# Performance work log

Hardware: AMD Instinct MI355X
Metric: run time of the kernel (lower is better)

The kernel has to match this reference:

```python
import jax, jax.numpy as jnp
import numpy as np

B, V, H, W = 1, 88, 128, 256
P = 2                  # patch size
D = 128                # hidden_dim = embed_dim // latent_ratio = 1536 // 12
NG = 12                # n_group (== latent_ratio)
NH = 2                 # heads per attention = num_heads // latent_ratio = 24 // 12
E = NG * D             # embed_dim = 1536
HD = D // NH
SCALE = HD ** -0.5

# Static ragged group index sets derived from the variable names (sizes 7,7,7,7,7,9,9,9,9,9,17,6).
# Pressure-level vars are ordered z,q,t,u,v per level; levels [50..400]=7 levels, [50..600]=9 levels.
_off = {'z': 0, 'q': 1, 't': 2, 'u': 3, 'v': 4}
GROUPS = []
for name in ['u1', 'v1', 't1', 'q1', 'z1', 'u2', 'v2', 't2', 'q2', 'z2', 'surf', 'const']:
    if name[-1] in '12':
        nl = 7 if name[-1] == '1' else 9
        GROUPS.append(np.array([5 * li + _off[name[0]] for li in range(nl)]))
    elif name == 'surf':
        GROUPS.append(np.arange(65, 82))   # 17 surface vars
    else:
        GROUPS.append(np.arange(82, 88))   # 6 constant vars


def setup_inputs() -> dict:
    key = jax.random.key(0)
    ks = jax.random.split(key, 16)
    return {
        "x": jax.random.normal(ks[0], (B, V, H, W), jnp.float32),
        # per-variable conv patch-embed weights, flattened to (V, P*P, D)
        "conv_w": jax.random.normal(ks[1], (V, P * P, D), jnp.float32) * 0.05,
        "conv_b": jax.random.normal(ks[2], (V, D), jnp.float32) * 0.02,
        "channel_embed": jax.random.normal(ks[3], (1, V, D), jnp.float32) * 0.02,
        "channel_query": jax.random.uniform(ks[4], (1, NG, D), jnp.float32) * 0.2,
        # 12 distinct MultiheadAttention modules: packed in_proj (3D, D) + out_proj
        "grp_in_w": jax.random.normal(ks[5], (NG, 3 * D, D), jnp.float32) * 0.05,
        "grp_in_b": jax.random.normal(ks[6], (NG, 3 * D), jnp.float32) * 0.02,
        "grp_out_w": jax.random.normal(ks[7], (NG, D, D), jnp.float32) * 0.05,
        "grp_out_b": jax.random.normal(ks[8], (NG, D), jnp.float32) * 0.02,
        "ens_query": jax.random.uniform(ks[9], (1, NG, D), jnp.float32) * 0.2,
        "ens_in_w": jax.random.normal(ks[10], (3 * D, D), jnp.float32) * 0.05,
        "ens_in_b": jax.random.normal(ks[11], (3 * D,), jnp.float32) * 0.02,
        "ens_out_w": jax.random.normal(ks[12], (D, D), jnp.float32) * 0.05,
        "ens_out_b": jax.random.normal(ks[13], (D,), jnp.float32) * 0.02,
        "ln_gamma": jnp.ones((E,), jnp.float32),
        "ln_beta": jnp.zeros((E,), jnp.float32),
    }


def reference(x, conv_w, conv_b, channel_embed, channel_query,
              grp_in_w, grp_in_b, grp_out_w, grp_out_b,
              ens_query, ens_in_w, ens_in_b, ens_out_w, ens_out_b,
              ln_gamma, ln_beta):
    b, v, h, w = x.shape
    hp, wp = h // P, w // P
    L = hp * wp
    # non-overlapping stride-P conv with 1 input channel == patchify + per-variable matmul
    patches = x.reshape(b, v, hp, P, wp, P).transpose(0, 1, 2, 4, 3, 5).reshape(b, v, L, P * P)
    xe = jnp.einsum('bvlp,vpd->bvld', patches, conv_w) + conv_b[None, :, None, :]
    xe = xe + channel_embed[:, :, None, :]                 # (B, V, L, D)
    xn = xe.transpose(0, 2, 1, 3).reshape(b * L, v, D)     # (N, V, D), N = B*L

    outs = []
    for i, ids in enumerate(GROUPS):                       # 12 fixed, structurally distinct groups
        kv = xn[:, ids, :]                                 # (N, g, D), ragged g
        Wq, Wk, Wv = grp_in_w[i, :D], grp_in_w[i, D:2 * D], grp_in_w[i, 2 * D:]
        bq, bk, bv = grp_in_b[i, :D], grp_in_b[i, D:2 * D], grp_in_b[i, 2 * D:]
        q = (channel_query[0, i] @ Wq.T + bq).reshape(NH, HD)
        k = (kv @ Wk.T + bk).reshape(-1, len(ids), NH, HD)
        vv = (kv @ Wv.T + bv).reshape(-1, len(ids), NH, HD)
        a = jax.nn.softmax(jnp.einsum('hd,nghd->nhg', q, k) * SCALE, axis=-1)
        o = jnp.einsum('nhg,nghd->nhd', a, vv).reshape(-1, D)
        outs.append(o @ grp_out_w[i].T + grp_out_b[i])
    out = jnp.stack(outs, axis=1)                          # (N, 12, D)

    Wq, Wk, Wv = ens_in_w[:D], ens_in_w[D:2 * D], ens_in_w[2 * D:]
    bq, bk, bv = ens_in_b[:D], ens_in_b[D:2 * D], ens_in_b[2 * D:]
    q = (ens_query[0] @ Wq.T + bq).reshape(NG, NH, HD)     # 12 ensemble query tokens
    k = (out @ Wk.T + bk).reshape(-1, NG, NH, HD)
    vv = (out @ Wv.T + bv).reshape(-1, NG, NH, HD)
    a = jax.nn.softmax(jnp.einsum('thd,nshd->nhts', q, k) * SCALE, axis=-1)
    r = jnp.einsum('nhts,nshd->nthd', a, vv).reshape(-1, NG, D)
    r = (r @ ens_out_w.T + ens_out_b).reshape(b, L, E)     # (B, L, embed_dim)

    mu = r.mean(axis=-1, keepdims=True)
    var = r.var(axis=-1, keepdims=True)
    return (r - mu) * jax.lax.rsqrt(var + 1e-5) * ln_gamma + ln_beta
```

## Files before the change

### kernel.cpp

```cpp
#include <hip/hip_runtime.h>


typedef __attribute__((ext_vector_type(8))) short short8;
typedef __attribute__((ext_vector_type(4))) float f32x4;

__constant__ int GOFF[13] = {0,7,14,21,28,35,44,53,62,71,80,97,103};
__constant__ int K5A[12]  = {35,35,35,35,35,45,45,45,45,45,85,30};
__constant__ int SLOTS3[12] = {3,3,3,3,3,3,3,3,3,3,6,2};
__constant__ int FOFFA[12] = {0,3,6,9,12,15,18,21,24,27,30,36};
__constant__ int GSLOT[103] = {
  3,8,13,18,23,28,33,
  4,9,14,19,24,29,34,
  2,7,12,17,22,27,32,
  1,6,11,16,21,26,31,
  0,5,10,15,20,25,30,
  3,8,13,18,23,28,33,38,43,
  4,9,14,19,24,29,34,39,44,
  2,7,12,17,22,27,32,37,42,
  1,6,11,16,21,26,31,36,41,
  0,5,10,15,20,25,30,35,40,
  45,46,47,48,49,50,51,52,53,54,55,56,57,58,59,60,61,
  62,63,64,65,66,67};
__constant__ int GIDX[103] = {
  0,0,0,0,0,0,0, 1,1,1,1,1,1,1, 2,2,2,2,2,2,2, 3,3,3,3,3,3,3, 4,4,4,4,4,4,4,
  5,5,5,5,5,5,5,5,5, 6,6,6,6,6,6,6,6,6, 7,7,7,7,7,7,7,7,7, 8,8,8,8,8,8,8,8,8,
  9,9,9,9,9,9,9,9,9,
  10,10,10,10,10,10,10,10,10,10,10,10,10,10,10,10,10,
  11,11,11,11,11,11};

constexpr int cSLOTS[12] = {3,3,3,3,3,3,3,3,3,3,6,2};
constexpr int cFOFFA[12] = {0,3,6,9,12,15,18,21,24,27,30,36};

#define QK_GRP 0
#define QK_ENS 3072
#define QB_GRP 6144
#define QB_ENS 6176
#define CGRP   6208
#define CENS   7744
#define CWQ_BYTE   43776
#define MPL_BYTE   50432
#define MEB_BYTE   1623296
#define QKEB_BYTE  1688832
#define FWS_BYTE   1697024

__device__ __forceinline__ float bf2f(unsigned short s) {
  return __uint_as_float(((unsigned)s) << 16);
}
__device__ __forceinline__ unsigned short f2bf(float f) {
  unsigned u = __float_as_uint(f);
  u += 0x7fffu + ((u >> 16) & 1u);
  return (unsigned short)(u >> 16);
}

__global__ void hwe_p1(const float* __restrict__ giw, const float* __restrict__ gib,
                       const float* __restrict__ gow, const float* __restrict__ gob,
                       const float* __restrict__ cq,  const float* __restrict__ eq,
                       const float* __restrict__ eiw, const float* __restrict__ eib,
                       const float* __restrict__ eow, const float* __restrict__ eob,
                       float* __restrict__ wsf, float* __restrict__ Mplain,
                       unsigned short* __restrict__ MeB, unsigned short* __restrict__ Fws) {
  int blk = blockIdx.x, tid = threadIdx.x;
  int wave = tid >> 6, lane = tid & 63;
  if (blk < 48) {
    __shared__ float qf[64];
    bool ens = blk >= 24;
    int bi = ens ? blk - 24 : blk;
    int i = bi >> 1, h = bi & 1;
    const float* W  = ens ? eiw : giw + i*49152;
    const float* bv = ens ? eib : gib + i*384;
    const float* qv = ens ? eq + i*128 : cq + i*128;
    for (int it = 0; it < 16; ++it) {
      int dp = it*4 + wave;
      const float* wrow = W + (h*64 + dp)*128;
      float acc = wrow[lane]*qv[lane] + wrow[lane+64]*qv[lane+64];
#pragma unroll
      for (int off = 32; off > 0; off >>= 1) acc += __shfl_down(acc, off);
      if (lane == 0) qf[dp] = acc + bv[h*64 + dp];
    }
    __syncthreads();
    if (tid < 128) {
      int e = tid;
      const float* Wk = W + (128 + h*64)*128 + e;
      float a0=0.f,a1=0.f,a2=0.f,a3=0.f;
      for (int dp = 0; dp < 64; dp += 4) {
        a0 += qf[dp+0] * Wk[(dp+0)*128];
        a1 += qf[dp+1] * Wk[(dp+1)*128];
        a2 += qf[dp+2] * Wk[(dp+2)*128];
        a3 += qf[dp+3] * Wk[(dp+3)*128];
      }
      wsf[(ens ? QK_ENS : QK_GRP) + bi*128 + e] = (a0+a1)+(a2+a3);
    }
    if (wave == 3) {
      float acc = qf[lane] * bv[128 + h*64 + lane];
#pragma unroll
      for (int off = 32; off > 0; off >>= 1) acc += __shfl_down(acc, off);
      if (lane == 0) wsf[(ens ? QB_ENS : QB_GRP) + bi] = acc;
    }
  } else if (blk < 1584) {
    int b2 = blk - 48;
    int gi = b2 >> 7, r = b2 & 127;
    int ep = tid, h = ep >> 7, e = ep & 127;
    const float* wo = gow + gi*16384 + r*128 + h*64;
    const float* wv = giw + gi*49152 + (256 + h*64)*128 + e;
    float a0=0.f,a1=0.f,a2=0.f,a3=0.f;
    for (int hd = 0; hd < 64; hd += 4) {
      a0 += wo[hd+0] * wv[(hd+0)*128];
      a1 += wo[hd+1] * wv[(hd+1)*128];
      a2 += wo[hd+2] * wv[(hd+2)*128];
      a3 += wo[hd+3] * wv[(hd+3)*128];
    }
    Mplain[(gi*128 + r)*256 + ep] = (a0+a1)+(a2+a3);
  } else if (blk < 1712) {
    int f2 = (blk - 1584)*256 + tid;
    int r = f2 >> 8, ep = f2 & 255;
    int h = ep >> 7, e = ep & 127;
    const float* wo = eow + r*128 + h*64;
    const float* wv = eiw + (256 + h*64)*128 + e;
    float a0=0.f,a1=0.f,a2=0.f,a3=0.f;
    for (int hd = 0; hd < 64; hd += 4) {
      a0 += wo[hd+0] * wv[(hd+0)*128];
      a1 += wo[hd+1] * wv[(hd+1)*128];
      a2 += wo[hd+2] * wv[(hd+2)*128];
      a3 += wo[hd+3] * wv[(hd+3)*128];
    }
    float acc = (a0+a1)+(a2+a3);
    int mt = r >> 4, lr = r & 15, kt = ep >> 5, q = (ep >> 3) & 3, j = ep & 7;
    MeB[((mt*8 + kt)*64 + (q*16 + lr))*8 + j] = f2bf(acc);
  } else if (blk < 2096) {
    int id = (blk - 1712)*4 + wave;
    int i = id >> 7, d = id & 127;
    const float* wrow = gow + i*16384 + d*128;
    const float* bvv = gib + i*384 + 256;
    float acc = wrow[lane]*bvv[lane] + wrow[lane+64]*bvv[lane+64];
#pragma unroll
    for (int off = 32; off > 0; off >>= 1) acc += __shfl_down(acc, off);
    if (lane == 0) wsf[CGRP + id] = acc + gob[i*128 + d];
  } else if (blk < 2128) {
    int d = (blk - 2096)*4 + wave;
    const float* wrow = eow + d*128;
    const float* bvv = eib + 256;
    float acc = wrow[lane]*bvv[lane] + wrow[lane+64]*bvv[lane+64];
#pragma unroll
    for (int off = 32; off > 0; off >>= 1) acc += __shfl_down(acc, off);
    if (lane == 0) wsf[CENS + d] = acc + eob[d];
  } else {
    int idx = (blk - 2128)*256 + tid;
    if (idx < 19456) ((uint4*)Fws)[idx] = (uint4){0,0,0,0};
  }
}

__global__ void hwe_p2(const float* __restrict__ cw, const float* __restrict__ cb,
                       const float* __restrict__ ce, const float* __restrict__ Mplain,
                       const float* __restrict__ wsf,
                       unsigned short* __restrict__ Fws,
                       unsigned short* __restrict__ qkeB, float* __restrict__ cwq) {
  int blk = blockIdx.x, tid = threadIdx.x;
  if (blk < 192) {
    __shared__ __align__(16) unsigned short M16[16*130];
    __shared__ __align__(16) unsigned short cwl[85*130];
    int gi = blk >> 4, h = (blk >> 3) & 1, mt = blk & 7;
    int go = GOFF[gi], K5 = K5A[gi], S = SLOTS3[gi];
    int r0 = mt*16;
    for (int idx = tid; idx < 2048; idx += 256) {
      int rr = idx >> 7, e = idx & 127;
      M16[rr*130 + e] = f2bf(Mplain[(gi*128 + r0 + rr)*256 + h*128 + e]);
    }
    for (int idx = tid; idx < K5*128; idx += 256) {
      int k = idx >> 7, e = idx & 127;
      int q = (k*205) >> 10;
      int pp = k - q*5;
      int s = GSLOT[go + q];
      int v = (s < 45) ? s : s + 20;
      float val = (pp < 4) ? cw[(v*4 + pp)*128 + e] : (cb[v*128 + e] + ce[v*128 + e]);
      cwl[k*130 + e] = f2bf(val);
    }
    __syncthreads();
    const unsigned* M32 = (const unsigned*)M16;
    const unsigned* C32 = (const unsigned*)cwl;
    for (int o = tid; o < 16*K5; o += 256) {
      int k = o >> 4, rr = o & 15;
      float acc = 0.f;
#pragma unroll 8
      for (int e2 = 0; e2 < 64; ++e2) {
        unsigned m = M32[rr*65 + e2];
        unsigned c = C32[k*65 + e2];
        acc += __uint_as_float(m << 16) * __uint_as_float(c << 16);
        acc += __uint_as_float(m & 0xffff0000u) * __uint_as_float(c & 0xffff0000u);
      }
      int kpp = h*K5 + k;
      int ktl = kpp >> 5;
      int addr = (FOFFA[gi]*8 + mt*S + ktl)*512 + ((kpp >> 3) & 3)*128 + rr*8 + (kpp & 7);
      Fws[addr] = f2bf(acc);
    }
  } else if (blk < 208) {
    int f4 = (blk - 192)*256 + tid;
    int lane = (f4 >> 3) & 63, j = f4 & 7;
    int th = ((f4 >> 11) & 1)*16 + (lane & 15);
    int kt = (f4 >> 9) & 3;
    float val = (th < 24) ? wsf[QK_ENS + th*128 + kt*32 + (lane >> 4)*8 + j] : 0.f;
    qkeB[f4] = f2bf(val);
  } else {
    int wid = (blk - 208)*4 + (tid >> 6);
    int lane = tid & 63;
    if (wid < 206) {
      int gg = wid >> 1, h = wid & 1;
      int gi = GIDX[gg];
      int s = GSLOT[gg];
      int v = (s < 45) ? s : s + 20;
      const float* qk = wsf + QK_GRP + (gi*2 + h)*128;
      float q0 = qk[lane], q1 = qk[lane + 64];
      float a[5];
#pragma unroll
      for (int pp = 0; pp < 4; ++pp)
        a[pp] = cw[(v*4 + pp)*128 + lane]*q0 + cw[(v*4 + pp)*128 + lane + 64]*q1;
      a[4] = (cb[v*128 + lane] + ce[v*128 + lane])*q0 +
             (cb[v*128 + lane + 64] + ce[v*128 + lane + 64])*q1;
#pragma unroll
      for (int off = 32; off > 0; off >>= 1)
#pragma unroll
        for (int kk = 0; kk < 5; ++kk) a[kk] += __shfl_down(a[kk], off);
      if (lane == 0) {
        float* o = cwq + (gg*2 + h)*8;
        o[0] = a[0]*0.125f; o[1] = a[1]*0.125f; o[2] = a[2]*0.125f; o[3] = a[3]*0.125f;
        o[4] = (a[4] + wsf[QB_GRP + gi*2 + h]) * 0.125f;
      }
    }
  }
}

__global__ __launch_bounds__(256, 3) void hwe_main(
    const float* __restrict__ x,
    const float* __restrict__ lgam, const float* __restrict__ lbet,
    const float* __restrict__ wsf,  const float* __restrict__ cwq,
    const unsigned short* __restrict__ Fws, const unsigned short* __restrict__ MeB,
    const unsigned short* __restrict__ qkeB,
    float* __restrict__ out) {
  __shared__ __align__(16) unsigned char smem[53632];
  unsigned short* xpB   = (unsigned short*)(smem);
  unsigned short* scb   = (unsigned short*)(smem + 4352);
  unsigned short* wpAll = (unsigned short*)(smem + 7680);
  unsigned short* Gl    = (unsigned short*)(smem);
  unsigned short* apB   = (unsigned short*)(smem + 20480);
  unsigned short* sce2  = (unsigned short*)(smem);
  unsigned short* outg2 = (unsigned short*)(smem + 28672);
  float*          stats = (float*)(smem + 53504);

  const int tid  = threadIdx.x;
  const int wave = tid >> 6;
  const int lane = tid & 63;
  const int quad = lane >> 4;
  const int l15  = lane & 15;

  const int hi   = blockIdx.x >> 4;
  const int wib  = (blockIdx.x & 15) << 3;
  const int nbase = hi*128 + wib;

  for (int idx = tid; idx < 1088; idx += 256) {
    int c2 = idx & 7, r = (idx >> 3) & 1, s = idx >> 4;
    int v = (s < 45) ? s : s + 20;
    const float2 xv = *(const float2*)(x + (v*128 + 2*hi + r)*256 + 2*wib + c2*2);
    unsigned pk = (unsigned)f2bf(xv.x) | ((unsigned)f2bf(xv.y) << 16);
    *(unsigned*)(xpB + (c2*68 + s)*4 + r*2) = pk;
  }
  if (tid < 64) ((unsigned*)outg2)[96*64 + tid] = 0u;
  __syncthreads();

  for (int idx = tid; idx < 1648; idx += 256) {
    int h = idx & 1, p = (idx >> 1) & 7, gg = idx >> 4;
    int s = GSLOT[gg];
    const float* c = cwq + (gg*2 + h)*8;
    const unsigned short* xr = xpB + (p*68 + s)*4;
    float acc = c[4] + bf2f(xr[0])*c[0] + bf2f(xr[1])*c[1]
                     + bf2f(xr[2])*c[2] + bf2f(xr[3])*c[3];
    scb[(p*2 + h)*104 + gg] = f2bf(acc);
  }
  __syncthreads();

  if (tid < 192) {
    int gi = tid % 12, h = (tid / 12) & 1, p = tid / 24;
    int go = GOFF[gi], G = GOFF[gi+1] - go;
    unsigned short* row = scb + (p*2 + h)*104 + go;
    float ev[17];
    float m = -1e30f;
#pragma unroll
    for (int g = 0; g < 17; ++g) {
      ev[g] = (g < G) ? bf2f(row[g]) : -1e30f;
      m = fmaxf(m, ev[g]);
    }
    float ssum = 0.f;
#pragma unroll
    for (int g = 0; g < 17; ++g) {
      float e = __expf(ev[g] - m);
      ev[g] = e;
      if (g < G) ssum += e;
    }
    float inv = 1.f / ssum;
#pragma unroll
    for (int g = 0; g < 17; ++g)
      if (g < G) row[g] = f2bf(ev[g] * inv);
  }
  __syncthreads();

#pragma unroll
  for (int hb = 0; hb < 2; ++hb) {
    const int nsl = hb ? 20 : 18;
    const int sbase = hb ? 18 : 0;

    short8 fA[6], fB[6];
    float4 cgA, cgB;
    auto fws_issue = [&](int I, short8 (&buf)[6], float4& cg) {
      int gi = hb*6 + (I >> 1);
      int S  = cSLOTS[gi];
      int mt = (I & 1)*4 + wave;
      const unsigned short* fp = Fws + (cFOFFA[gi]*8 + mt*S)*512 + lane*8;
#pragma unroll
      for (int kt = 0; kt < 6; ++kt)
        if (kt < S) buf[kt] = *(const short8*)(fp + kt*512);
      cg = *(const float4*)(wsf + CGRP + gi*128 + mt*16 + quad*4);
    };
    auto fws_compute = [&](int I, short8 (&buf)[6], const float4& cg) {
      int gi = hb*6 + (I >> 1);
      int S  = cSLOTS[gi];
      int mt = (I & 1)*4 + wave;
      int lbase = cFOFFA[gi] - sbase;
      f32x4 acc = {0.f,0.f,0.f,0.f};
#pragma unroll
      for (int kt = 0; kt < 6; ++kt)
        if (kt < S) {
          short8 b = *(const short8*)(wpAll + (lbase + kt)*512 + lane*8);
          acc = __builtin_amdgcn_mfma_f32_16x16x32_bf16(buf[kt], b, acc, 0, 0, 0);
        }
      if (l15 < 8) {
        int p = l15;
        int rb = mt*16 + quad*4;
        unsigned short t0 = f2bf(acc[0] + cg.x);
        unsigned short t1 = f2bf(acc[1] + cg.y);
        unsigned short t2 = f2bf(acc[2] + cg.z);
        unsigned short t3 = f2bf(acc[3] + cg.w);
        uint2 w;
        w.x = (unsigned)t0 | ((unsigned)t1 << 16);
        w.y = (unsigned)t2 | ((unsigned)t3 << 16);
        int row = gi*8 + p;
        int ch = (rb >> 3) ^ ((gi ^ p) & 7);
        *(uint2*)(outg2 + row*128 + ch*8 + (rb & 7)) = w;
      }
    };

    fws_issue(0, fA, cgA);

    {
      const int nposs = nsl * 512;
      for (int pos = tid*4; pos < nposs; pos += 1024) {
        int pf = (pos >> 3) & 15;
        uint2 w2 = {0u, 0u};
        if (pf < 8) {
          int ls = pos >> 9;
          int qd = (pos >> 7) & 3;
          int j0 = pos & 7;
          int p  = pf;
          int gil, K5, fo, goffB, c0, stp;
          if (hb == 0) {
            gil = (ls>=3)+(ls>=6)+(ls>=9)+(ls>=12)+(ls>=15);
            K5 = (gil < 5) ? 35 : 45;
            fo = gil*3;
            goffB = gil*7;
            c0 = (gil==0)?3:(gil==1)?4:(gil==2)?2:(gil==3)?1:(gil==4)?0:3;
            stp = 5;
          } else {
            gil = (ls>=3)+(ls>=6)+(ls>=9)+(ls>=12)+(ls>=18);
            K5 = (gil < 4) ? 45 : (gil == 4) ? 85 : 30;
            fo = (gil < 5) ? gil*3 : 18;
            goffB = (gil < 5) ? (44 + gil*9) : 97;
            c0 = (gil==0)?4:(gil==1)?2:(gil==2)?1:(gil==3)?0:(gil==4)?45:62;
            stp = (gil < 4) ? 5 : 1;
          }
          int kbase = (ls - fo)*32 + qd*8 + j0;
          unsigned short vv[4];
#pragma unroll
          for (int jj = 0; jj < 4; ++jj) {
            int kpp = kbase + jj;
            int h = (kpp >= K5) ? 1 : 0;
            int k = kpp - (h ? K5 : 0);
            int q = (k*205) >> 10;
            int pp = k - q*5;
            int gg = goffB + q;
            int s = c0 + q*stp;
            float a  = bf2f(scb[(p*2 + h)*104 + gg]);
            float xv = bf2f(xpB[(p*68 + s)*4 + pp]);
            float val = (pp < 4) ? a * xv : a;
            if (kpp >= 2*K5) val = 0.f;
            vv[jj] = f2bf(val);
          }
          w2.x = (unsigned)vv[0] | ((unsigned)vv[1] << 16);
          w2.y = (unsigned)vv[2] | ((unsigned)vv[3] << 16);
        }
        *(uint2*)(wpAll + pos) = w2;
      }
    }
    __syncthreads();

#pragma unroll
    for (int ii = 0; ii < 6; ++ii) {
      fws_issue(ii*2 + 1, fB, cgB);
      fws_compute(ii*2, fA, cgA);
      if (ii < 5) fws_issue(ii*2 + 2, fA, cgA);
      fws_compute(ii*2 + 1, fB, cgB);
    }
    __syncthreads();
  }

#pragma unroll
  for (int ti = 0; ti < 3; ++ti) {
    int T = wave*3 + ti;
    int mtp = T >> 1, ntp = T & 1;
    int rowA = mtp*16 + l15;
    int sx = ((rowA >> 3) ^ rowA) & 7;
    f32x4 acc = {0.f,0.f,0.f,0.f};
#pragma unroll
    for (int kt = 0; kt < 4; ++kt) {
      short8 a = *(const short8*)(outg2 + rowA*128 + (((kt*4 + quad) ^ sx) << 3));
      short8 b = *(const short8*)(qkeB + ((ntp*4 + kt)*64 + lane)*8);
      acc = __builtin_amdgcn_mfma_f32_16x16x32_bf16(a, b, acc, 0, 0, 0);
    }
    int th = ntp*16 + l15;
    if (th < 24) {
      float qb = wsf[QB_ENS + th];
#pragma unroll
      for (int reg = 0; reg < 4; ++reg) {
        int rowE = mtp*16 + quad*4 + reg;
        sce2[((rowE & 7)*24 + th)*16 + (rowE >> 3)] = f2bf((acc[reg] + qb) * 0.125f);
      }
    }
  }
  __syncthreads();

  if (tid < 192) {
    unsigned short* row = sce2 + tid*16;
    float ev[12];
    float m = -1e30f;
#pragma unroll
    for (int s = 0; s < 12; ++s) { ev[s] = bf2f(row[s]); m = fmaxf(m, ev[s]); }
    float ssum = 0.f;
#pragma unroll
    for (int s = 0; s < 12; ++s) { float e = __expf(ev[s] - m); ev[s] = e; ssum += e; }
    float inv = 1.f / ssum;
#pragma unroll
    for (int s = 0; s < 12; ++s) row[s] = f2bf(ev[s] * inv);
  }
  __syncthreads();

  for (int idx = tid; idx < 4096; idx += 256) {
    int p = idx >> 9, r9 = idx & 511;
    int ln = r9 >> 3, j = r9 & 7;
    int t = ln & 15, qd = ln >> 4;
    int kpp = qd*8 + j;
    int h = kpp >> 4, s = kpp & 15;
    unsigned short v = 0;
    if (s < 12 && t < 12) v = sce2[(p*24 + t*2 + h)*16 + s];
    apB[p*512 + ln*8 + j] = v;
  }
  float cens0[4], cens1[4];
  {
    float4 c0 = *(const float4*)(wsf + CENS + (wave*2 + 0)*16 + quad*4);
    float4 c1 = *(const float4*)(wsf + CENS + (wave*2 + 1)*16 + quad*4);
    cens0[0]=c0.x; cens0[1]=c0.y; cens0[2]=c0.z; cens0[3]=c0.w;
    cens1[0]=c1.x; cens1[1]=c1.y; cens1[2]=c1.z; cens1[3]=c1.w;
  }
  short8 meAr[16];
#pragma unroll
  for (int mi = 0; mi < 2; ++mi)
#pragma unroll
    for (int h = 0; h < 2; ++h)
#pragma unroll
      for (int kt = 0; kt < 4; ++kt)
        meAr[(mi*2 + h)*4 + kt] =
          *(const short8*)(MeB + (((wave*2 + mi)*8 + h*4 + kt)*64 + lane)*8);
  __syncthreads();

  for (int pp2 = 0; pp2 < 4; ++pp2) {
    f32x4 g[2][2][2];
#pragma unroll
    for (int lp = 0; lp < 2; ++lp)
#pragma unroll
      for (int mi = 0; mi < 2; ++mi)
#pragma unroll
        for (int h = 0; h < 2; ++h) g[lp][mi][h] = (f32x4){0.f,0.f,0.f,0.f};
#pragma unroll
    for (int lp = 0; lp < 2; ++lp) {
      int p = pp2*2 + lp;
      int brow = (l15 < 12) ? (l15*8 + p) : 96;
      int sx = ((brow >> 3) ^ brow) & 7;
#pragma unroll
      for (int h = 0; h < 2; ++h) {
#pragma unroll
        for (int kt = 0; kt < 4; ++kt) {
          short8 b = *(const short8*)(outg2 + brow*128 + (((kt*4 + quad) ^ sx) << 3));
          g[lp][0][h] = __builtin_amdgcn_mfma_f32_16x16x32_bf16(
              meAr[(0*2 + h)*4 + kt], b, g[lp][0][h], 0, 0, 0);
          g[lp][1][h] = __builtin_amdgcn_mfma_f32_16x16x32_bf16(
              meAr[(1*2 + h)*4 + kt], b, g[lp][1][h], 0, 0, 0);
        }
      }
    }
#pragma unroll
    for (int lp = 0; lp < 2; ++lp)
#pragma unroll
      for (int mi = 0; mi < 2; ++mi)
#pragma unroll
        for (int h = 0; h < 2; ++h)
#pragma unroll
          for (int reg = 0; reg < 4; ++reg) {
            int r = (wave*2 + mi)*16 + quad*4 + reg;
            Gl[lp*5120 + r*40 + h*16 + l15] = f2bf(g[lp][mi][h][reg]);
          }

    f32x4 rr[2][2];
    float s1[2] = {0.f, 0.f}, s2[2] = {0.f, 0.f};
#pragma unroll
    for (int lp = 0; lp < 2; ++lp) {
      int p = pp2*2 + lp;
      short8 bfrag = *(const short8*)(apB + p*512 + lane*8);
#pragma unroll
      for (int mi = 0; mi < 2; ++mi) {
        int mt2 = wave*2 + mi;
        short8 afrag = *(const short8*)(Gl + lp*5120 + (mt2*16 + l15)*40 + quad*8);
        f32x4 acc = {0.f,0.f,0.f,0.f};
        acc = __builtin_amdgcn_mfma_f32_16x16x32_bf16(afrag, bfrag, acc, 0, 0, 0);
#pragma unroll
        for (int reg = 0; reg < 4; ++reg)
          acc[reg] += (mi ? cens1[reg] : cens0[reg]);
        rr[lp][mi] = acc;
        if (l15 < 12) {
#pragma unroll
          for (int reg = 0; reg < 4; ++reg) {
            float v = acc[reg];
            s1[lp] += v; s2[lp] += v*v;
          }
        }
      }
    }
#pragma unroll
    for (int off = 32; off > 0; off >>= 1) {
#pragma unroll
      for (int lp = 0; lp < 2; ++lp) {
        s1[lp] += __shfl_xor(s1[lp], off);
        s2[lp] += __shfl_xor(s2[lp], off);
      }
    }
    int sb = (pp2 & 1) << 4;
    if (lane == 0) {
#pragma unroll
      for (int lp = 0; lp < 2; ++lp) {
        stats[sb + lp*4 + wave] = s1[lp];
        stats[sb + 8 + lp*4 + wave] = s2[lp];
      }
    }
    __syncthreads();
#pragma unroll
    for (int lp = 0; lp < 2; ++lp) {
      float t1 = stats[sb+lp*4+0] + stats[sb+lp*4+1] + stats[sb+lp*4+2] + stats[sb+lp*4+3];
      float t2 = stats[sb+8+lp*4+0] + stats[sb+8+lp*4+1] + stats[sb+8+lp*4+2] + stats[sb+8+lp*4+3];
      float mean = t1 * (1.f/1536.f);
      float var  = t2 * (1.f/1536.f) - mean*mean;
      float rstd = rsqrtf(var + 1e-5f);
      if (l15 < 12) {
        long nrow = (long)(nbase + pp2*2 + lp) * 1536;
#pragma unroll
        for (int mi = 0; mi < 2; ++mi) {
          int rb = (wave*2 + mi)*16 + quad*4;
          int j = l15*128 + rb;
          float4 gm = *(const float4*)(lgam + j);
          float4 bt = *(const float4*)(lbet + j);
          float4 o;
          o.x = (rr[lp][mi][0] - mean)*rstd*gm.x + bt.x;
          o.y = (rr[lp][mi][1] - mean)*rstd*gm.y + bt.y;
          o.z = (rr[lp][mi][2] - mean)*rstd*gm.z + bt.z;
          o.w = (rr[lp][mi][3] - mean)*rstd*gm.w + bt.w;
          *(float4*)(out + nrow + j) = o;
        }
      }
    }
  }
}

extern "C" void kernel_launch(void* const* d_in, const int* in_sizes, int n_in,
                              void* d_out, int out_size, void* d_ws, size_t ws_size,
                              hipStream_t stream) {
  const float* x   = (const float*)d_in[0];
  const float* cw  = (const float*)d_in[1];
  const float* cb  = (const float*)d_in[2];
  const float* ce  = (const float*)d_in[3];
  const float* cq  = (const float*)d_in[4];
  const float* giw = (const float*)d_in[5];
  const float* gib = (const float*)d_in[6];
  const float* gow = (const float*)d_in[7];
  const float* gob = (const float*)d_in[8];
  const float* eq  = (const float*)d_in[9];
  const float* eiw = (const float*)d_in[10];
  const float* eib = (const float*)d_in[11];
  const float* eow = (const float*)d_in[12];
  const float* eob = (const float*)d_in[13];
  const float* lg  = (const float*)d_in[14];
  const float* lb  = (const float*)d_in[15];

  float* wsf = (float*)d_ws;
  float* cwq = (float*)((char*)d_ws + CWQ_BYTE);
  float* Mplain = (float*)((char*)d_ws + MPL_BYTE);
  unsigned short* MeB  = (unsigned short*)((char*)d_ws + MEB_BYTE);
  unsigned short* qkeB = (unsigned short*)((char*)d_ws + QKEB_BYTE);
  unsigned short* Fws  = (unsigned short*)((char*)d_ws + FWS_BYTE);

  hwe_p1<<<2204, 256, 0, stream>>>(giw, gib, gow, gob, cq, eq, eiw, eib, eow, eob,
                                   wsf, Mplain, MeB, Fws);
  hwe_p2<<<260, 256, 0, stream>>>(cw, cb, ce, Mplain, wsf, Fws, qkeB, cwq);
  hwe_main<<<1024, 256, 0, stream>>>(x, lg, lb, wsf, cwq, Fws, MeB, qkeB,
                                     (float*)d_out);
}
```

Baseline: 205.1 us.

## Compute fused weight product in p2 with bf16 MFMA using pre-swizzled operands

The first kernel now writes the Wo·Wv product directly as bf16 in an MFMA-fragment layout and packs the gathered conv weights and biases into bf16 B-tiles. The second kernel then replaces its LDS staging and scalar bf16 dot-product loop with 16x16x32 bf16 MFMA instructions reading those tiles straight from global memory. This removes shared-memory staging, the barrier and scalar FMA work in the weight-folding stage, in exchange for 38 extra blocks in the first kernel. The main kernel, which likely dominates total time, is unchanged.

```diff
diff --git a/kernel.cpp b/kernel.cpp
--- a/kernel.cpp
+++ b/kernel.cpp
@@ -27,6 +27,10 @@
   9,9,9,9,9,9,9,9,9,
   10,10,10,10,10,10,10,10,10,10,10,10,10,10,10,10,10,
   11,11,11,11,11,11};
+__constant__ int TGI[38] = {0,0,0,1,1,1,2,2,2,3,3,3,4,4,4,5,5,5,6,6,6,7,7,7,
+                            8,8,8,9,9,9,10,10,10,10,10,10,11,11};
+__constant__ int TNT[38] = {0,1,2,0,1,2,0,1,2,0,1,2,0,1,2,0,1,2,0,1,2,0,1,2,
+                            0,1,2,0,1,2,0,1,2,3,4,5,0,1};
 
 constexpr int cSLOTS[12] = {3,3,3,3,3,3,3,3,3,3,6,2};
 constexpr int cFOFFA[12] = {0,3,6,9,12,15,18,21,24,27,30,36};
@@ -39,6 +43,7 @@
 #define CENS   7744
 #define CWQ_BYTE   43776
 #define MPL_BYTE   50432
+#define CW2_BYTE   836864
 #define MEB_BYTE   1623296
 #define QKEB_BYTE  1688832
 #define FWS_BYTE   1697024
@@ -57,7 +62,10 @@
                        const float* __restrict__ cq,  const float* __restrict__ eq,
                        const float* __restrict__ eiw, const float* __restrict__ eib,
                        const float* __restrict__ eow, const float* __restrict__ eob,
-                       float* __restrict__ wsf, float* __restrict__ Mplain,
+                       const float* __restrict__ cw,  const float* __restrict__ cb,
+                       const float* __restrict__ ce,
+                       float* __restrict__ wsf, unsigned short* __restrict__ MA,
+                       unsigned short* __restrict__ CW2,
                        unsigned short* __restrict__ MeB, unsigned short* __restrict__ Fws) {
   int blk = blockIdx.x, tid = threadIdx.x;
   int wave = tid >> 6, lane = tid & 63;
@@ -109,7 +117,9 @@
       a2 += wo[hd+2] * wv[(hd+2)*128];
       a3 += wo[hd+3] * wv[(hd+3)*128];
     }
-    Mplain[(gi*128 + r)*256 + ep] = (a0+a1)+(a2+a3);
+    float acc = (a0+a1)+(a2+a3);
+    int mt = r >> 4, lr = r & 15, kt = e >> 5, q = (e >> 3) & 3, j = e & 7;
+    MA[(((gi*2 + h)*8 + mt)*4 + kt)*512 + (q*16 + lr)*8 + j] = f2bf(acc);
   } else if (blk < 1712) {
     int f2 = (blk - 1584)*256 + tid;
     int r = f2 >> 8, ep = f2 & 255;
@@ -143,65 +153,89 @@
 #pragma unroll
     for (int off = 32; off > 0; off >>= 1) acc += __shfl_down(acc, off);
     if (lane == 0) wsf[CENS + d] = acc + eob[d];
+  } else if (blk < 2166) {
+    int tile = blk - 2128;
+    int gi = TGI[tile], nt = TNT[tile];
+    int kt = tid >> 6;
+    int l15b = tid & 15, quadb = (tid >> 4) & 3;
+    int k = nt*16 + l15b;
+    int e = kt*32 + quadb*8;
+    unsigned short vv[8];
+    if (k < K5A[gi]) {
+      int q = (k*205) >> 10;
+      int pp = k - q*5;
+      int s = GSLOT[GOFF[gi] + q];
+      int v = (s < 45) ? s : s + 20;
+      if (pp < 4) {
+        const float* src = cw + (v*4 + pp)*128 + e;
+#pragma unroll
+        for (int j = 0; j < 8; ++j) vv[j] = f2bf(src[j]);
+      } else {
+        const float* b1 = cb + v*128 + e;
+        const float* c1 = ce + v*128 + e;
+#pragma unroll
+        for (int j = 0; j < 8; ++j) vv[j] = f2bf(b1[j] + c1[j]);
+      }
+    } else {
+#pragma unroll
+      for (int j = 0; j < 8; ++j) vv[j] = 0;
+    }
+    unsigned short* dst = CW2 + (tile*4 + kt)*512 + (tid & 63)*8;
+#pragma unroll
+    for (int j = 0; j < 8; ++j) dst[j] = vv[j];
   } else {
-    int idx = (blk - 2128)*256 + tid;
+    int idx = (blk - 2166)*256 + tid;
     if (idx < 19456) ((uint4*)Fws)[idx] = (uint4){0,0,0,0};
   }
 }
 
 __global__ void hwe_p2(const float* __restrict__ cw, const float* __restrict__ cb,
-                       const float* __restrict__ ce, const float* __restrict__ Mplain,
+                       const float* __restrict__ ce,
+                       const unsigned short* __restrict__ MA,
+                       const unsigned short* __restrict__ CW2,
                        const float* __restrict__ wsf,
                        unsigned short* __restrict__ Fws,
                        unsigned short* __restrict__ qkeB, float* __restrict__ cwq) {
   int blk = blockIdx.x, tid = threadIdx.x;
+  int wave = tid >> 6, lane = tid & 63;
+  int quad = lane >> 4, l15 = lane & 15;
   if (blk < 192) {
-    __shared__ __align__(16) unsigned short M16[16*130];
-    __shared__ __align__(16) unsigned short cwl[85*130];
     int gi = blk >> 4, h = (blk >> 3) & 1, mt = blk & 7;
-    int go = GOFF[gi], K5 = K5A[gi], S = SLOTS3[gi];
-    int r0 = mt*16;
-    for (int idx = tid; idx < 2048; idx += 256) {
-      int rr = idx >> 7, e = idx & 127;
-      M16[rr*130 + e] = f2bf(Mplain[(gi*128 + r0 + rr)*256 + h*128 + e]);
-    }
-    for (int idx = tid; idx < K5*128; idx += 256) {
-      int k = idx >> 7, e = idx & 127;
-      int q = (k*205) >> 10;
-      int pp = k - q*5;
-      int s = GSLOT[go + q];
-      int v = (s < 45) ? s : s + 20;
-      float val = (pp < 4) ? cw[(v*4 + pp)*128 + e] : (cb[v*128 + e] + ce[v*128 + e]);
-      cwl[k*130 + e] = f2bf(val);
-    }
-    __syncthreads();
-    const unsigned* M32 = (const unsigned*)M16;
-    const unsigned* C32 = (const unsigned*)cwl;
-    for (int o = tid; o < 16*K5; o += 256) {
-      int k = o >> 4, rr = o & 15;
-      float acc = 0.f;
-#pragma unroll 8
-      for (int e2 = 0; e2 < 64; ++e2) {
-        unsigned m = M32[rr*65 + e2];
-        unsigned c = C32[k*65 + e2];
-        acc += __uint_as_float(m << 16) * __uint_as_float(c << 16);
-        acc += __uint_as_float(m & 0xffff0000u) * __uint_as_float(c & 0xffff0000u);
-      }
-      int kpp = h*K5 + k;
-      int ktl = kpp >> 5;
-      int addr = (FOFFA[gi]*8 + mt*S + ktl)*512 + ((kpp >> 3) & 3)*128 + rr*8 + (kpp & 7);
-      Fws[addr] = f2bf(acc);
+    int K5 = K5A[gi], S = SLOTS3[gi];
+    const unsigned short* MAp = MA + (((gi*2 + h)*8 + mt)*4)*512 + lane*8;
+    short8 a[4];
+#pragma unroll
+    for (int kt = 0; kt < 4; ++kt)
+      a[kt] = *(const short8*)(MAp + kt*512);
+    for (int nt = wave; nt < S; nt += 4) {
+      const unsigned short* Bp = CW2 + (FOFFA[gi] + nt)*2048 + lane*8;
+      f32x4 acc = {0.f,0.f,0.f,0.f};
+#pragma unroll
+      for (int kt = 0; kt < 4; ++kt) {
+        short8 b = *(const short8*)(Bp + kt*512);
+        acc = __builtin_amdgcn_mfma_f32_16x16x32_bf16(a[kt], b, acc, 0, 0, 0);
+      }
+      int k = nt*16 + l15;
+      if (k < K5) {
+        int kpp = h*K5 + k;
+        int base = (FOFFA[gi]*8 + mt*S + (kpp >> 5))*512
+                 + ((kpp >> 3) & 3)*128 + (kpp & 7);
+#pragma unroll
+        for (int reg = 0; reg < 4; ++reg) {
+          int rr = quad*4 + reg;
+          Fws[base + rr*8] = f2bf(acc[reg]);
+        }
+      }
     }
   } else if (blk < 208) {
     int f4 = (blk - 192)*256 + tid;
-    int lane = (f4 >> 3) & 63, j = f4 & 7;
-    int th = ((f4 >> 11) & 1)*16 + (lane & 15);
+    int ln = (f4 >> 3) & 63, j = f4 & 7;
+    int th = ((f4 >> 11) & 1)*16 + (ln & 15);
     int kt = (f4 >> 9) & 3;
-    float val = (th < 24) ? wsf[QK_ENS + th*128 + kt*32 + (lane >> 4)*8 + j] : 0.f;
+    float val = (th < 24) ? wsf[QK_ENS + th*128 + kt*32 + (ln >> 4)*8 + j] : 0.f;
     qkeB[f4] = f2bf(val);
   } else {
-    int wid = (blk - 208)*4 + (tid >> 6);
-    int lane = tid & 63;
+    int wid = (blk - 208)*4 + wave;
     if (wid < 206) {
       int gg = wid >> 1, h = wid & 1;
       int gi = GIDX[gg];
@@ -605,14 +639,15 @@
 
   float* wsf = (float*)d_ws;
   float* cwq = (float*)((char*)d_ws + CWQ_BYTE);
-  float* Mplain = (float*)((char*)d_ws + MPL_BYTE);
+  unsigned short* MA   = (unsigned short*)((char*)d_ws + MPL_BYTE);
+  unsigned short* CW2  = (unsigned short*)((char*)d_ws + CW2_BYTE);
   unsigned short* MeB  = (unsigned short*)((char*)d_ws + MEB_BYTE);
   unsigned short* qkeB = (unsigned short*)((char*)d_ws + QKEB_BYTE);
   unsigned short* Fws  = (unsigned short*)((char*)d_ws + FWS_BYTE);
 
-  hwe_p1<<<2204, 256, 0, stream>>>(giw, gib, gow, gob, cq, eq, eiw, eib, eow, eob,
-                                   wsf, Mplain, MeB, Fws);
-  hwe_p2<<<260, 256, 0, stream>>>(cw, cb, ce, Mplain, wsf, Fws, qkeB, cwq);
+  hwe_p1<<<2242, 256, 0, stream>>>(giw, gib, gow, gob, cq, eq, eiw, eib, eow, eob,
+                                   cw, cb, ce, wsf, MA, CW2, MeB, Fws);
+  hwe_p2<<<260, 256, 0, stream>>>(cw, cb, ce, MA, CW2, wsf, Fws, qkeB, cwq);
   hwe_main<<<1024, 256, 0, stream>>>(x, lg, lb, wsf, cwq, Fws, MeB, qkeB,
                                      (float*)d_out);
 }
```

Measured after the change: 177.6 us. 1.15x faster.
